# Kernel tuning notes

Measured on AMD Instinct MI355X. Metric: run time of the kernel, lower is better.

## Reference

```python
import jax, jax.numpy as jnp
import numpy as np

SINKHORN_ITERS = 4
EPS = 1e-6


def setup_inputs() -> dict:
    key = jax.random.key(0)
    B, T, W, D = 2, 4096, 4, 2048
    k1, k2 = jax.random.split(key, 2)
    x = jax.random.normal(k1, (B, T, W, D), dtype=jnp.float32)
    W_router = jax.random.normal(k2, (W * W + 2 * W, D), dtype=jnp.float32) * 0.02
    b_router = jnp.zeros((W * W + 2 * W,), dtype=jnp.float32)
    return {"x": x, "W_router": W_router, "b_router": b_router}


def _sinkhorn(logits):
    # Bistochastic projection: 4 iterations of alternating row/col normalization.
    def body(w, _):
        w = w / jnp.maximum(w.sum(axis=-1, keepdims=True), EPS)
        w = w / jnp.maximum(w.sum(axis=-2, keepdims=True), EPS)
        return w, None
    w, _ = jax.lax.scan(body, jnp.exp(logits), None, length=SINKHORN_ITERS)
    return w


def reference(x, W_router, b_router):
    B, T, W, D = x.shape
    # router input: mean over the width (stream) dim -> (B, T, D)
    routing_input = x.mean(axis=2)
    raw = routing_input @ W_router.T + b_router          # (B, T, W*W + 2W)
    pre = jax.nn.softmax(raw[..., :W], axis=-1)          # (B, T, W)
    post = jax.nn.softmax(raw[..., W:2 * W], axis=-1)    # (B, T, W)
    res_logits = raw[..., 2 * W:].reshape(B, T, W, W)
    # residual_bias buffer: -2 off-diagonal, +2 on diagonal
    idx = jnp.arange(W)
    bias = jnp.full((W, W), -2.0, dtype=x.dtype).at[idx, idx].set(2.0)
    residual = _sinkhorn(res_logits + bias)              # (B, T, W, W)
    # aggregate streams with pre weights, apply op (identity here)
    aggregated = (x * pre[..., None]).sum(axis=2)        # (B, T, D)
    op_out = aggregated                                  # op = identity
    mixed_residual = jnp.einsum('btij,btjd->btid', residual, x)
    return mixed_residual + post[..., None] * op_out[:, :, None, :]
```

## Files before the change

### kernel.cpp

```cpp
#include <hip/hip_runtime.h>


#define SINKHORN_ITERS 4
#define EPSV 1e-6f

typedef float f32x4 __attribute__((ext_vector_type(4)));

__global__ __launch_bounds__(256, 4) void mchc_fused(
    const float* __restrict__ x,
    const float* __restrict__ Wr,
    const float* __restrict__ br,
    float* __restrict__ out)
{
    const int token = blockIdx.x;
    const int tid   = threadIdx.x;
    const int lane  = tid & 63;
    const int wave  = tid >> 6;

    const f32x4* __restrict__ x4 = (const f32x4*)(x + (size_t)token * 8192);
    const f32x4* __restrict__ w4 = (const f32x4*)Wr;
    f32x4*       __restrict__ o4 = (f32x4*)(out + (size_t)token * 8192);

    __shared__ f32x4 xs[8][256];
    __shared__ float red[4][24];
    __shared__ float rawbuf[24];
    __shared__ float Mbuf[16];

    f32x4 xa[4], xb[4];
#pragma unroll
    for (int w = 0; w < 4; ++w) {
        xa[w] = x4[w * 512 + tid];
        xb[w] = x4[w * 512 + 256 + tid];
    }
    f32x4 wa[8], wb[8];
#pragma unroll
    for (int r = 0; r < 8; ++r) {
        wa[r] = w4[r * 512 + tid];
        wb[r] = w4[r * 512 + 256 + tid];
    }
    __builtin_amdgcn_sched_barrier(0);

    f32x4 sa = xa[0] + xa[1] + xa[2] + xa[3];
    f32x4 sb = xb[0] + xb[1] + xb[2] + xb[3];

#pragma unroll
    for (int w = 0; w < 4; ++w) {
        xs[w][tid]     = xa[w];
        xs[4 + w][tid] = xb[w];
    }
    __builtin_amdgcn_sched_barrier(0);

    float p[24];
#pragma unroll
    for (int g = 0; g < 3; ++g) {
        if (g > 0) {
#pragma unroll
            for (int r = 0; r < 8; ++r) {
                wa[r] = w4[(g * 8 + r) * 512 + tid];
                wb[r] = w4[(g * 8 + r) * 512 + 256 + tid];
            }
            __builtin_amdgcn_sched_barrier(0);
        }
#pragma unroll
        for (int r = 0; r < 8; ++r) {
            f32x4 t = sa * wa[r] + sb * wb[r];
            p[g * 8 + r] = t.x + t.y + t.z + t.w;
        }
    }

#pragma unroll
    for (int k = 0; k < 24; ++k) {
        float v = p[k];
        v += __shfl_xor(v, 1);
        v += __shfl_xor(v, 2);
        v += __shfl_xor(v, 4);
        v += __shfl_xor(v, 8);
        v += __shfl_xor(v, 16);
        v += __shfl_xor(v, 32);
        p[k] = v;
    }
    if (lane == 0) {
#pragma unroll
        for (int k = 0; k < 24; ++k) red[wave][k] = p[k];
    }
    __syncthreads();

    if (tid < 24) {
        float r = red[0][tid] + red[1][tid] + red[2][tid] + red[3][tid];
        rawbuf[tid] = 0.25f * r + br[tid];
    }
    __syncthreads();

    if (tid < 16) {
        const int i = tid >> 2, j = tid & 3;

        float r0 = rawbuf[0], r1 = rawbuf[1], r2 = rawbuf[2], r3 = rawbuf[3];
        float mp = fmaxf(fmaxf(r0, r1), fmaxf(r2, r3));
        float sp = __expf(r0 - mp) + __expf(r1 - mp) + __expf(r2 - mp) + __expf(r3 - mp);
        float pre_j = __expf(rawbuf[j] - mp) / sp;

        float q0 = rawbuf[4], q1 = rawbuf[5], q2 = rawbuf[6], q3 = rawbuf[7];
        float mq = fmaxf(fmaxf(q0, q1), fmaxf(q2, q3));
        float sq = __expf(q0 - mq) + __expf(q1 - mq) + __expf(q2 - mq) + __expf(q3 - mq);
        float post_i = __expf(rawbuf[4 + i] - mq) / sq;

        float w = __expf(rawbuf[8 + tid] + ((i == j) ? 2.0f : -2.0f));
#pragma unroll
        for (int it = 0; it < SINKHORN_ITERS; ++it) {
            float rs = w + __shfl_xor(w, 1);
            rs += __shfl_xor(rs, 2);
            w /= fmaxf(rs, EPSV);
            float cs = w + __shfl_xor(w, 4);
            cs += __shfl_xor(cs, 8);
            w /= fmaxf(cs, EPSV);
        }
        Mbuf[tid] = w + post_i * pre_j;
    }
    __syncthreads();

    float M[16];
#pragma unroll
    for (int m = 0; m < 16; ++m) M[m] = Mbuf[m];

    f32x4 ya[4], yb[4];
#pragma unroll
    for (int w = 0; w < 4; ++w) {
        ya[w] = xs[w][tid];
        yb[w] = xs[4 + w][tid];
    }

#pragma unroll
    for (int i = 0; i < 4; ++i) {
        const float m0 = M[i * 4 + 0], m1 = M[i * 4 + 1];
        const float m2 = M[i * 4 + 2], m3 = M[i * 4 + 3];
        f32x4 oa = m0 * ya[0] + m1 * ya[1] + m2 * ya[2] + m3 * ya[3];
        f32x4 ob = m0 * yb[0] + m1 * yb[1] + m2 * yb[2] + m3 * yb[3];
        o4[i * 512 + tid]       = oa;
        o4[i * 512 + 256 + tid] = ob;
    }
}

extern "C" void kernel_launch(void* const* d_in, const int* in_sizes, int n_in,
                              void* d_out, int out_size, void* d_ws, size_t ws_size,
                              hipStream_t stream) {
    const float* x  = (const float*)d_in[0];
    const float* Wr = (const float*)d_in[1];
    const float* br = (const float*)d_in[2];
    float* out = (float*)d_out;

    const int tokens = in_sizes[0] / (4 * 2048);
    mchc_fused<<<dim3(tokens), dim3(256), 0, stream>>>(x, Wr, br, out);
}
```

Baseline: 515.9 us.

## Stream router weights through LDS via direct global-to-LDS loads

Router weight rows are no longer loaded into registers. They are now copied in chunks of two rows straight into shared memory with global_load_lds, and the dot products read them from LDS. The loop runs 12 chunks with a single buffer and two barriers per chunk, and the launch-bounds occupancy hint drops from 4 to 3. The intent is to cut register pressure and let the weight fetch bypass VGPRs. The risks are serialized load/compute from the single buffer, many extra barriers, and reduced occupancy. Correctness of the direct-to-LDS path also relies on vmcnt waits that __syncthreads does not obviously provide.

```diff
diff --git a/kernel.cpp b/kernel.cpp
--- a/kernel.cpp
+++ b/kernel.cpp
@@ -6,7 +6,14 @@
 
 typedef float f32x4 __attribute__((ext_vector_type(4)));
 
-__global__ __launch_bounds__(256, 4) void mchc_fused(
+__device__ __forceinline__ void gload_lds16(const float* g, float* l) {
+    __builtin_amdgcn_global_load_lds(
+        (const __attribute__((address_space(1))) void*)g,
+        (__attribute__((address_space(3))) void*)l,
+        16, 0, 0);
+}
+
+__global__ __launch_bounds__(256, 3) void mchc_fused(
     const float* __restrict__ x,
     const float* __restrict__ Wr,
     const float* __restrict__ br,
@@ -18,9 +25,9 @@
     const int wave  = tid >> 6;
 
     const f32x4* __restrict__ x4 = (const f32x4*)(x + (size_t)token * 8192);
-    const f32x4* __restrict__ w4 = (const f32x4*)Wr;
     f32x4*       __restrict__ o4 = (f32x4*)(out + (size_t)token * 8192);
 
+    __shared__ float wlds[4096];
     __shared__ f32x4 xs[8][256];
     __shared__ float red[4][24];
     __shared__ float rawbuf[24];
@@ -32,13 +39,13 @@
         xa[w] = x4[w * 512 + tid];
         xb[w] = x4[w * 512 + 256 + tid];
     }
-    f32x4 wa[8], wb[8];
+    {
+        const float* g = Wr + wave * 1024 + lane * 4;
+        float*       l = wlds + wave * 1024;
 #pragma unroll
-    for (int r = 0; r < 8; ++r) {
-        wa[r] = w4[r * 512 + tid];
-        wb[r] = w4[r * 512 + 256 + tid];
+        for (int i = 0; i < 4; ++i)
+            gload_lds16(g + i * 256, l + i * 256);
     }
-    __builtin_amdgcn_sched_barrier(0);
 
     f32x4 sa = xa[0] + xa[1] + xa[2] + xa[3];
     f32x4 sb = xb[0] + xb[1] + xb[2] + xb[3];
@@ -48,23 +55,25 @@
         xs[w][tid]     = xa[w];
         xs[4 + w][tid] = xb[w];
     }
-    __builtin_amdgcn_sched_barrier(0);
 
     float p[24];
 #pragma unroll
-    for (int g = 0; g < 3; ++g) {
-        if (g > 0) {
+    for (int c = 0; c < 12; ++c) {
+        __syncthreads();
 #pragma unroll
-            for (int r = 0; r < 8; ++r) {
-                wa[r] = w4[(g * 8 + r) * 512 + tid];
-                wb[r] = w4[(g * 8 + r) * 512 + 256 + tid];
-            }
-            __builtin_amdgcn_sched_barrier(0);
+        for (int r = 0; r < 2; ++r) {
+            f32x4 wa = *(const f32x4*)&wlds[r * 2048 + tid * 4];
+            f32x4 wb = *(const f32x4*)&wlds[r * 2048 + 1024 + tid * 4];
+            f32x4 t = sa * wa + sb * wb;
+            p[c * 2 + r] = t.x + t.y + t.z + t.w;
         }
+        __syncthreads();
+        if (c < 11) {
+            const float* g = Wr + (c + 1) * 4096 + wave * 1024 + lane * 4;
+            float*       l = wlds + wave * 1024;
 #pragma unroll
-        for (int r = 0; r < 8; ++r) {
-            f32x4 t = sa * wa[r] + sb * wb[r];
-            p[g * 8 + r] = t.x + t.y + t.z + t.w;
+            for (int i = 0; i < 4; ++i)
+                gload_lds16(g + i * 256, l + i * 256);
         }
     }
 
```

Result: faster. 504.6 us (-2.2%).
